# Kernel optimization log

Measured on AMD Instinct MI355X. Metric: run time of the kernel, lower is better.

Reference implementation:

```python
import jax, jax.numpy as jnp
import numpy as np

N_NODES = 100000
N_EDGES = 600000
IN_CH = 128
HID = 64
N_REL = 8


def setup_inputs() -> dict:
    key = jax.random.key(0)
    ks = jax.random.split(key, 9)
    x = jax.random.normal(ks[0], (N_NODES, IN_CH), dtype=jnp.float32)
    edge_index = jax.random.randint(ks[1], (2, N_EDGES), 0, N_NODES)
    edge_type = jax.random.randint(ks[2], (N_EDGES,), 0, N_REL)
    s_in = 1.0 / np.sqrt(IN_CH)   # torch Linear init bound
    s_h = 1.0 / np.sqrt(HID)
    W_rel = jax.random.uniform(ks[3], (N_REL, HID, IN_CH), minval=-s_in, maxval=s_in, dtype=jnp.float32)
    b_rel = jax.random.uniform(ks[4], (N_REL, HID), minval=-s_in, maxval=s_in, dtype=jnp.float32)
    W_self = jax.random.uniform(ks[5], (HID, IN_CH), minval=-s_in, maxval=s_in, dtype=jnp.float32)
    b_self = jax.random.uniform(ks[6], (HID,), minval=-s_in, maxval=s_in, dtype=jnp.float32)
    W_out = jax.random.uniform(ks[7], (1, HID), minval=-s_h, maxval=s_h, dtype=jnp.float32)
    b_out = jax.random.uniform(ks[8], (1,), minval=-s_h, maxval=s_h, dtype=jnp.float32)
    return {"x": x, "edge_index": edge_index, "edge_type": edge_type,
            "W_rel": W_rel, "b_rel": b_rel, "W_self": W_self, "b_self": b_self,
            "W_out": W_out, "b_out": b_out}


def reference(x, edge_index, edge_type, W_rel, b_rel, W_self, b_self, W_out, b_out):
    row, col = edge_index[0], edge_index[1]
    R, H, _ = W_rel.shape
    N = x.shape[0]
    # Project every node under every relation once ([R, N, H]) instead of the
    # per-relation masked gather->GEMM loop: same math (sum over edges of
    # W_{edge_type} x_{src} + b_{edge_type} scattered into dst).
    xp = jnp.einsum('ni,rhi->rnh', x, W_rel)                     # [R, N, H]
    msg = xp.reshape(R * N, H)[edge_type * N + row] + b_rel[edge_type]  # [E, H]
    agg = jax.ops.segment_sum(msg, col, num_segments=N)          # scatter-add into dst
    out = jax.nn.relu(agg + x @ W_self.T + b_self)               # [N, H]
    return (out @ W_out.T + b_out)[:, 0]                          # [N]
```

## Files before the change

kernel.cpp:

```cpp
#include <hip/hip_runtime.h>
#include <hip/hip_bf16.h>

#define IN_CH    128
#define HID      64
#define N_REL    8
#define ZCH      576
#define SLOT_CAP 32
#define NBKT     784
#define BKT_CAP  1024
#define ZBLK     128
#define ZSROW    584

using bf16x8 = __attribute__((ext_vector_type(8))) short;
using f32x4  = __attribute__((ext_vector_type(4))) float;

__device__ __forceinline__ short f2bf(float f) {
    unsigned int u = __float_as_uint(f);
    u += 0x7fffu + ((u >> 16) & 1u);
    return (short)(u >> 16);
}

__global__ __launch_bounds__(1024) void prep0_kernel(
    const float* __restrict__ W_rel, const float* __restrict__ W_self,
    unsigned short* __restrict__ wpk2, unsigned int* __restrict__ gcount)
{
    const int b = blockIdx.x, tid = threadIdx.x;
    if (b < 9) {
        int gid  = b * 1024 + tid;
        int kt   = gid / 2304;
        int rem  = gid - kt * 2304;
        int mt   = rem >> 6;
        int lane = rem & 63;
        int ch   = mt * 16 + (lane & 15);
        int k0   = kt * 32 + ((lane >> 4) << 3);
        bf16x8 o;
        #pragma unroll
        for (int j = 0; j < 8; ++j) {
            int k = k0 + j;
            float v = (ch < 512)
                ? W_rel[(size_t)(ch >> 6) * (HID * IN_CH) + (size_t)(ch & 63) * IN_CH + k]
                : W_self[(size_t)(ch - 512) * IN_CH + k];
            o[j] = f2bf(v);
        }
        *(bf16x8*)(wpk2 + (size_t)gid * 8) = o;
    } else {
        if (tid < NBKT) gcount[tid] = 0u;
    }
}

__global__ __launch_bounds__(1024) void k1_kernel(
    const int* __restrict__ edge_index, const int* __restrict__ edge_type,
    unsigned int* __restrict__ gcount, uint2* __restrict__ gbuf, int E, int nbB,
    const float* __restrict__ x, const unsigned short* __restrict__ wpk2,
    unsigned short* __restrict__ z, int N)
{
    __shared__ unsigned int hist[NBKT];
    __shared__ short xs[ZBLK * 136];
    __shared__ short zs[16 * ZSROW];
    const int b = blockIdx.x, tid = threadIdx.x;
    if (b < nbB) {
        for (int i = tid; i < NBKT; i += 1024) hist[i] = 0u;
        __syncthreads();
        const int e0 = (b * 1024 + tid) * 8;
        unsigned int pay[8]; unsigned int dstv[8]; unsigned int rnk[8]; int bkt[8];
        const bool full = (e0 + 8 <= E);
        if (full) {
            int4 s0 = *(const int4*)(edge_index + e0);
            int4 s1 = *(const int4*)(edge_index + e0 + 4);
            int4 d0 = *(const int4*)(edge_index + E + e0);
            int4 d1 = *(const int4*)(edge_index + E + e0 + 4);
            int4 t0 = *(const int4*)(edge_type + e0);
            int4 t1 = *(const int4*)(edge_type + e0 + 4);
            const int* sp0 = &s0.x; const int* sp1 = &s1.x;
            const int* dp0 = &d0.x; const int* dp1 = &d1.x;
            const int* tp0 = &t0.x; const int* tp1 = &t1.x;
            #pragma unroll
            for (int j = 0; j < 4; ++j) {
                pay[j]     = (unsigned int)sp0[j] * 1152u
                           + ((unsigned int)tp0[j] << 7) + ((unsigned int)tp0[j] << 28);
                dstv[j]    = (unsigned int)dp0[j];
                pay[j + 4] = (unsigned int)sp1[j] * 1152u
                           + ((unsigned int)tp1[j] << 7) + ((unsigned int)tp1[j] << 28);
                dstv[j + 4]= (unsigned int)dp1[j];
            }
            #pragma unroll
            for (int j = 0; j < 8; ++j) {
                bkt[j] = (int)(dstv[j] >> 7);
                rnk[j] = atomicAdd(&hist[bkt[j]], 1u);
            }
        }
        __syncthreads();
        for (int bb = tid; bb < NBKT; bb += 1024) {
            unsigned int c = hist[bb];
            if (c) hist[bb] = atomicAdd(&gcount[bb], c);
        }
        __syncthreads();
        if (full) {
            #pragma unroll
            for (int j = 0; j < 8; ++j) {
                unsigned int p = hist[bkt[j]] + rnk[j];
                if (p < BKT_CAP) {
                    uint2 v; v.x = pay[j]; v.y = dstv[j];
                    gbuf[(size_t)bkt[j] * BKT_CAP + p] = v;
                }
            }
        }
    } else {
        const int nodebase = (b - nbB) * ZBLK;
        {
            int node = tid >> 3;
            int ch0  = (tid & 7) * 16;
            int ng   = nodebase + node;
            if (ng < N) {
                const float* p = x + (size_t)ng * IN_CH + ch0;
                float4 a0 = *(const float4*)p;
                float4 a1 = *(const float4*)(p + 4);
                float4 a2 = *(const float4*)(p + 8);
                float4 a3 = *(const float4*)(p + 12);
                bf16x8 o0, o1;
                o0[0]=f2bf(a0.x); o0[1]=f2bf(a0.y); o0[2]=f2bf(a0.z); o0[3]=f2bf(a0.w);
                o0[4]=f2bf(a1.x); o0[5]=f2bf(a1.y); o0[6]=f2bf(a1.z); o0[7]=f2bf(a1.w);
                o1[0]=f2bf(a2.x); o1[1]=f2bf(a2.y); o1[2]=f2bf(a2.z); o1[3]=f2bf(a2.w);
                o1[4]=f2bf(a3.x); o1[5]=f2bf(a3.y); o1[6]=f2bf(a3.z); o1[7]=f2bf(a3.w);
                *(bf16x8*)(xs + node * 136 + ch0)     = o0;
                *(bf16x8*)(xs + node * 136 + ch0 + 8) = o1;
            }
        }
        __syncthreads();
        const int wave = tid >> 6, lane = tid & 63;
        const int l16 = lane & 15, q = lane >> 4;
        const bf16x8* wv = (const bf16x8*)wpk2;
        char* zsb = (char*)zs;
        for (int nt = 0; nt < 8; ++nt) {
            if (nodebase + nt * 16 >= N) break;
            const short* abase = xs + (nt * 16 + l16) * 136 + (q << 3);
            bf16x8 afrag[4];
            #pragma unroll
            for (int kt = 0; kt < 4; ++kt)
                afrag[kt] = *(const bf16x8*)(abase + kt * 32);

            auto do_mt = [&](int mt) {
                f32x4 acc = {0.f, 0.f, 0.f, 0.f};
                #pragma unroll
                for (int kt = 0; kt < 4; ++kt) {
                    bf16x8 wf = wv[(size_t)((kt * 36 + mt) * 64) + lane];
                    acc = __builtin_amdgcn_mfma_f32_16x16x32_bf16(
                        wf, afrag[kt], acc, 0, 0, 0);
                }
                uint2 v;
                v.x = ((unsigned int)(unsigned short)f2bf(acc[1]) << 16)
                    | (unsigned int)(unsigned short)f2bf(acc[0]);
                v.y = ((unsigned int)(unsigned short)f2bf(acc[3]) << 16)
                    | (unsigned int)(unsigned short)f2bf(acc[2]);
                *(uint2*)(zsb + l16 * (ZSROW * 2) + mt * 32 + (q << 3)) = v;
            };
            do_mt(wave);
            do_mt(wave + 16);
            if (wave < 4) do_mt(wave + 32);
            __syncthreads();
            {
                char* dst = (char*)(z + (size_t)(nodebase + nt * 16) * ZCH);
                #pragma unroll
                for (int p = 0; p < 2; ++p) {
                    int li = p * 1024 + tid;
                    if (li < 1152) {
                        int node = li / 72;
                        int rem  = li - node * 72;
                        uint4 vv = *(const uint4*)(zsb + node * (ZSROW * 2) + rem * 16);
                        *(uint4*)(dst + (size_t)li * 16) = vv;
                    }
                }
            }
            __syncthreads();
        }
    }
}

__global__ __launch_bounds__(256) void k2_kernel(
    const unsigned int* __restrict__ gcount, const uint2* __restrict__ gbuf,
    int* __restrict__ cnt, unsigned int* __restrict__ slots, int N)
{
    __shared__ unsigned int hist[128];
    const int b = blockIdx.x, tid = threadIdx.x;
    if (tid < 128) hist[tid] = 0u;
    __syncthreads();
    unsigned int bc = gcount[b]; if (bc > BKT_CAP) bc = BKT_CAP;
    for (unsigned int i = tid; i < bc; i += 256) {
        uint2 v = gbuf[(size_t)b * BKT_CAP + i];
        unsigned int d = v.y;
        unsigned int r = atomicAdd(&hist[d & 127], 1u);
        if (r < SLOT_CAP) slots[(size_t)d * SLOT_CAP + r] = v.x;
    }
    __syncthreads();
    if (tid < 128) {
        int d = b * 128 + tid;
        if (d < N) cnt[d] = (int)hist[tid];
    }
}

__global__ __launch_bounds__(256) void agg_kernel(
    const unsigned short* __restrict__ z, const int* __restrict__ cnt,
    const unsigned int* __restrict__ slots,
    const float* __restrict__ b_rel, const float* __restrict__ b_self,
    const float* __restrict__ W_out, const float* __restrict__ b_out,
    float* __restrict__ out, int N)
{
    const int tid  = threadIdx.x;
    const int g    = blockIdx.x * 4 + (tid >> 6);
    const int lane = tid & 63;

    const int rawdeg = cnt[g];
    unsigned int ev = 0u;
    if (lane < SLOT_CAP) ev = slots[(size_t)g * SLOT_CAP + lane];
    const float selfv =
        __uint_as_float((unsigned int)z[(size_t)g * ZCH + 512 + lane] << 16);

    const int deg = (rawdeg > SLOT_CAP) ? SLOT_CAP : rawdeg;
    const int myr = (lane < deg) ? (int)(ev >> 28) : 8;
    int cr[8];
    #pragma unroll
    for (int r = 0; r < 8; ++r) cr[r] = (int)__popcll(__ballot(myr == r));

    const char* zb = (const char*)z;
    float agg = 0.f;
    for (int e0 = 0; e0 < deg; e0 += 8) {
        int bn = deg - e0; if (bn > 8) bn = 8;
        unsigned int sv[8]; unsigned short gv[8];
        #pragma unroll
        for (int i = 0; i < 8; ++i) {
            if (i < bn) {
                sv[i] = (unsigned int)__builtin_amdgcn_readlane((int)ev, e0 + i);
                gv[i] = *(const unsigned short*)(zb + (sv[i] & 0x0FFFFFFFu) + (lane << 1));
            }
        }
        #pragma unroll
        for (int i = 0; i < 8; ++i) {
            if (i >= bn) break;
            agg += __uint_as_float((unsigned int)gv[i] << 16);
        }
    }

    float h = agg + selfv + b_self[lane];
    #pragma unroll
    for (int r = 0; r < 8; ++r)
        h += (float)cr[r] * b_rel[r * HID + lane];
    h = fmaxf(h, 0.f) * W_out[lane];
    #pragma unroll
    for (int m = 32; m >= 1; m >>= 1)
        h += __shfl_xor(h, m, 64);
    if (lane == 0) out[g] = h + b_out[0];
}

extern "C" void kernel_launch(void* const* d_in, const int* in_sizes, int n_in,
                              void* d_out, int out_size, void* d_ws, size_t ws_size,
                              hipStream_t stream)
{
    const float* x          = (const float*)d_in[0];
    const int*   edge_index = (const int*)  d_in[1];
    const int*   edge_type  = (const int*)  d_in[2];
    const float* W_rel      = (const float*)d_in[3];
    const float* b_rel      = (const float*)d_in[4];
    const float* W_self     = (const float*)d_in[5];
    const float* b_self     = (const float*)d_in[6];
    const float* W_out      = (const float*)d_in[7];
    const float* b_out      = (const float*)d_in[8];
    float* out = (float*)d_out;

    const int N = in_sizes[0] / IN_CH;
    const int E = in_sizes[2];

    char* w = (char*)d_ws;
    unsigned short* wpk2 = (unsigned short*)w; w += 147456;
    int* cnt             = (int*)w;            w += ((size_t)N * 4 + 255) & ~255ull;
    unsigned int* slots  = (unsigned int*)w;   w += (size_t)N * SLOT_CAP * 4;
    unsigned int* gcount = (unsigned int*)w;   w += (NBKT * 4 + 255) & ~255;
    uint2* gbuf          = (uint2*)w;          w += (size_t)NBKT * BKT_CAP * 8;
    unsigned short* z    = (unsigned short*)w; w += (size_t)N * ZCH * 2;

    const int nbB     = (E + 8191) / 8192;
    const int zblocks = (N + ZBLK - 1) / ZBLK;

    prep0_kernel<<<10, 1024, 0, stream>>>(W_rel, W_self, wpk2, gcount);

    k1_kernel<<<nbB + zblocks, 1024, 0, stream>>>(
        edge_index, edge_type, gcount, gbuf, E, nbB, x, wpk2, z, N);

    k2_kernel<<<NBKT, 256, 0, stream>>>(gcount, gbuf, cnt, slots, N);

    agg_kernel<<<N / 4, 256, 0, stream>>>(
        z, cnt, slots, b_rel, b_self, W_out, b_out, out, N);
}
```

Baseline: 223.5 us.

## Fuse bucket scatter into aggregation kernel and double-buffer z staging

Merges the k2 bucket-to-slot kernel and the aggregation kernel into one kernel. Per-destination slot lists are built in shared memory and consumed right away, instead of going through a global slots/cnt array. This removes one launch and a large global write and re-read of slot data. It also double-buffers the z staging tile in the projection kernel to drop one barrier per node tile. The fused kernel runs only 782 blocks of 1024 threads, each wave handling 8 nodes in sequence, which lowers the parallelism available to hide gather latency.

```diff
diff --git a/kernel.cpp b/kernel.cpp
--- a/kernel.cpp
+++ b/kernel.cpp
@@ -56,7 +56,7 @@
 {
     __shared__ unsigned int hist[NBKT];
     __shared__ short xs[ZBLK * 136];
-    __shared__ short zs[16 * ZSROW];
+    __shared__ short zs[2][16 * ZSROW];
     const int b = blockIdx.x, tid = threadIdx.x;
     if (b < nbB) {
         for (int i = tid; i < NBKT; i += 1024) hist[i] = 0u;
@@ -130,7 +130,7 @@
         const int wave = tid >> 6, lane = tid & 63;
         const int l16 = lane & 15, q = lane >> 4;
         const bf16x8* wv = (const bf16x8*)wpk2;
-        char* zsb = (char*)zs;
+        int cur = 0;
         for (int nt = 0; nt < 8; ++nt) {
             if (nodebase + nt * 16 >= N) break;
             const short* abase = xs + (nt * 16 + l16) * 136 + (q << 3);
@@ -138,6 +138,7 @@
             #pragma unroll
             for (int kt = 0; kt < 4; ++kt)
                 afrag[kt] = *(const bf16x8*)(abase + kt * 32);
+            char* zsb = (char*)zs[cur];
 
             auto do_mt = [&](int mt) {
                 f32x4 acc = {0.f, 0.f, 0.f, 0.f};
@@ -171,84 +172,79 @@
                     }
                 }
             }
-            __syncthreads();
-        }
-    }
-}
-
-__global__ __launch_bounds__(256) void k2_kernel(
+            cur ^= 1;
+        }
+    }
+}
+
+__global__ __launch_bounds__(1024) void k2agg_kernel(
     const unsigned int* __restrict__ gcount, const uint2* __restrict__ gbuf,
-    int* __restrict__ cnt, unsigned int* __restrict__ slots, int N)
+    const unsigned short* __restrict__ z,
+    const float* __restrict__ b_rel, const float* __restrict__ b_self,
+    const float* __restrict__ W_out, const float* __restrict__ b_out,
+    float* __restrict__ out, int N)
 {
     __shared__ unsigned int hist[128];
+    __shared__ unsigned int slotbuf[128 * SLOT_CAP];
     const int b = blockIdx.x, tid = threadIdx.x;
     if (tid < 128) hist[tid] = 0u;
     __syncthreads();
     unsigned int bc = gcount[b]; if (bc > BKT_CAP) bc = BKT_CAP;
-    for (unsigned int i = tid; i < bc; i += 256) {
+    for (unsigned int i = tid; i < bc; i += 1024) {
         uint2 v = gbuf[(size_t)b * BKT_CAP + i];
-        unsigned int d = v.y;
-        unsigned int r = atomicAdd(&hist[d & 127], 1u);
-        if (r < SLOT_CAP) slots[(size_t)d * SLOT_CAP + r] = v.x;
+        unsigned int ln = v.y & 127u;
+        unsigned int r = atomicAdd(&hist[ln], 1u);
+        if (r < SLOT_CAP) slotbuf[ln * SLOT_CAP + r] = v.x;
     }
     __syncthreads();
-    if (tid < 128) {
-        int d = b * 128 + tid;
-        if (d < N) cnt[d] = (int)hist[tid];
-    }
-}
-
-__global__ __launch_bounds__(256) void agg_kernel(
-    const unsigned short* __restrict__ z, const int* __restrict__ cnt,
-    const unsigned int* __restrict__ slots,
-    const float* __restrict__ b_rel, const float* __restrict__ b_self,
-    const float* __restrict__ W_out, const float* __restrict__ b_out,
-    float* __restrict__ out, int N)
-{
-    const int tid  = threadIdx.x;
-    const int g    = blockIdx.x * 4 + (tid >> 6);
-    const int lane = tid & 63;
-
-    const int rawdeg = cnt[g];
-    unsigned int ev = 0u;
-    if (lane < SLOT_CAP) ev = slots[(size_t)g * SLOT_CAP + lane];
-    const float selfv =
-        __uint_as_float((unsigned int)z[(size_t)g * ZCH + 512 + lane] << 16);
-
-    const int deg = (rawdeg > SLOT_CAP) ? SLOT_CAP : rawdeg;
-    const int myr = (lane < deg) ? (int)(ev >> 28) : 8;
-    int cr[8];
+
+    const int wave = tid >> 6, lane = tid & 63;
+    const char* zb = (const char*)z;
     #pragma unroll
-    for (int r = 0; r < 8; ++r) cr[r] = (int)__popcll(__ballot(myr == r));
-
-    const char* zb = (const char*)z;
-    float agg = 0.f;
-    for (int e0 = 0; e0 < deg; e0 += 8) {
-        int bn = deg - e0; if (bn > 8) bn = 8;
-        unsigned int sv[8]; unsigned short gv[8];
-        #pragma unroll
-        for (int i = 0; i < 8; ++i) {
-            if (i < bn) {
-                sv[i] = (unsigned int)__builtin_amdgcn_readlane((int)ev, e0 + i);
-                gv[i] = *(const unsigned short*)(zb + (sv[i] & 0x0FFFFFFFu) + (lane << 1));
-            }
-        }
-        #pragma unroll
-        for (int i = 0; i < 8; ++i) {
-            if (i >= bn) break;
-            agg += __uint_as_float((unsigned int)gv[i] << 16);
-        }
-    }
-
-    float h = agg + selfv + b_self[lane];
-    #pragma unroll
-    for (int r = 0; r < 8; ++r)
-        h += (float)cr[r] * b_rel[r * HID + lane];
-    h = fmaxf(h, 0.f) * W_out[lane];
-    #pragma unroll
-    for (int m = 32; m >= 1; m >>= 1)
-        h += __shfl_xor(h, m, 64);
-    if (lane == 0) out[g] = h + b_out[0];
+    for (int i = 0; i < 8; ++i) {
+        const int ln = wave * 8 + i;
+        const int g  = b * 128 + ln;
+        if (g >= N) break;
+        int deg = (int)hist[ln];
+        if (deg > SLOT_CAP) deg = SLOT_CAP;
+        unsigned int ev = 0u;
+        if (lane < deg) ev = slotbuf[ln * SLOT_CAP + lane];
+        const float selfv =
+            __uint_as_float((unsigned int)z[(size_t)g * ZCH + 512 + lane] << 16);
+
+        const int myr = (lane < deg) ? (int)(ev >> 28) : 8;
+        int cr[8];
+        #pragma unroll
+        for (int r = 0; r < 8; ++r) cr[r] = (int)__popcll(__ballot(myr == r));
+
+        float agg = 0.f;
+        for (int e0 = 0; e0 < deg; e0 += 8) {
+            int bn = deg - e0; if (bn > 8) bn = 8;
+            unsigned int sv[8]; unsigned short gv[8];
+            #pragma unroll
+            for (int j = 0; j < 8; ++j) {
+                if (j < bn) {
+                    sv[j] = (unsigned int)__builtin_amdgcn_readlane((int)ev, e0 + j);
+                    gv[j] = *(const unsigned short*)(zb + (sv[j] & 0x0FFFFFFFu) + (lane << 1));
+                }
+            }
+            #pragma unroll
+            for (int j = 0; j < 8; ++j) {
+                if (j >= bn) break;
+                agg += __uint_as_float((unsigned int)gv[j] << 16);
+            }
+        }
+
+        float h = agg + selfv + b_self[lane];
+        #pragma unroll
+        for (int r = 0; r < 8; ++r)
+            h += (float)cr[r] * b_rel[r * HID + lane];
+        h = fmaxf(h, 0.f) * W_out[lane];
+        #pragma unroll
+        for (int m = 32; m >= 1; m >>= 1)
+            h += __shfl_xor(h, m, 64);
+        if (lane == 0) out[g] = h + b_out[0];
+    }
 }
 
 extern "C" void kernel_launch(void* const* d_in, const int* in_sizes, int n_in,
@@ -271,8 +267,6 @@
 
     char* w = (char*)d_ws;
     unsigned short* wpk2 = (unsigned short*)w; w += 147456;
-    int* cnt             = (int*)w;            w += ((size_t)N * 4 + 255) & ~255ull;
-    unsigned int* slots  = (unsigned int*)w;   w += (size_t)N * SLOT_CAP * 4;
     unsigned int* gcount = (unsigned int*)w;   w += (NBKT * 4 + 255) & ~255;
     uint2* gbuf          = (uint2*)w;          w += (size_t)NBKT * BKT_CAP * 8;
     unsigned short* z    = (unsigned short*)w; w += (size_t)N * ZCH * 2;
@@ -285,8 +279,6 @@
     k1_kernel<<<nbB + zblocks, 1024, 0, stream>>>(
         edge_index, edge_type, gcount, gbuf, E, nbB, x, wpk2, z, N);
 
-    k2_kernel<<<NBKT, 256, 0, stream>>>(gcount, gbuf, cnt, slots, N);
-
-    agg_kernel<<<N / 4, 256, 0, stream>>>(
-        z, cnt, slots, b_rel, b_self, W_out, b_out, out, N);
-}
+    k2agg_kernel<<<zblocks, 1024, 0, stream>>>(
+        gcount, gbuf, z, b_rel, b_self, W_out, b_out, out, N);
+}
```

New measurement: 214.1 us. -4.2%, faster.
